# Kernel optimization log

Hardware: AMD Instinct MI355X
Metric: run time of the kernel (lower is better)

The kernel has to match this reference:

```python
import jax, jax.numpy as jnp
import numpy as np

HEAD = 16

def setup_inputs() -> dict:
    key = jax.random.key(0)
    k1, k2, k3 = jax.random.split(key, 3)
    B, S, D = 2, 2048, 1024
    x = jax.random.normal(k1, (B, S, D), dtype=jnp.float32)
    w_qkv = jax.random.normal(k2, (D, 3 * D), dtype=jnp.float32) * (1.0 / np.sqrt(D))
    b_qkv = jnp.zeros((3 * D,), dtype=jnp.float32)
    w_out = jax.random.normal(k3, (D, D), dtype=jnp.float32) * (1.0 / np.sqrt(D))
    b_out = jnp.zeros((D,), dtype=jnp.float32)
    return {"x": x, "w_qkv": w_qkv, "b_qkv": b_qkv, "w_out": w_out, "b_out": b_out}


def reference(x, w_qkv, b_qkv, w_out, b_out):
    B, S, D = x.shape
    hd = D // HEAD  # head dim
    qkv = x @ w_qkv + b_qkv                      # [B,S,3D]
    qkv = qkv.reshape(B, S, 3, HEAD, hd)
    qkv = jnp.transpose(qkv, (2, 0, 3, 1, 4))    # [3,B,H,S,hd]
    q, k, v = qkv[0], qkv[1], qkv[2]
    scores = jnp.einsum('bhqd,bhkd->bhqk', q, k)  # [B,H,S,S]
    causal = jnp.triu(jnp.ones((S, S), dtype=bool), k=1)
    scores = jnp.where(causal, -jnp.inf, scores)
    scores = scores / jnp.sqrt(jnp.asarray(hd, dtype=x.dtype))
    attn = jax.nn.softmax(scores, axis=-1)
    z = jnp.einsum('bhqk,bhkd->bhqd', attn, v)   # [B,H,S,hd]
    z = jnp.transpose(z, (0, 2, 1, 3)).reshape(B, S, D)
    out = z @ w_out + b_out
    return out
```

## Files before the change

kernel.cpp:

```cpp
#include <hip/hip_runtime.h>

#define S_LEN  2048
#define NH     16
#define HD     64
#define DMODEL 1024

using bf16x8 = __attribute__((ext_vector_type(8))) __bf16;
using f32x4  = __attribute__((ext_vector_type(4))) float;

__device__ __forceinline__ unsigned short f2bf(float f) {
    unsigned u = __float_as_uint(f);
    u += 0x7FFFu + ((u >> 16) & 1u);
    return (unsigned short)(u >> 16);
}
__device__ __forceinline__ unsigned pk_trunc(float lo, float hi) {
    return __builtin_amdgcn_perm(__float_as_uint(hi), __float_as_uint(lo), 0x07060302u);
}

#define EXP2(x) __builtin_amdgcn_exp2f(x)

#define GLDS16(gsrc, ldst) \
    __builtin_amdgcn_global_load_lds((__attribute__((address_space(1))) void*)(gsrc), \
                                     (__attribute__((address_space(3))) void*)(ldst), 16, 0, 0)

#define WAIT_LGKM0() __builtin_amdgcn_s_waitcnt(0xC07F)

#define ASM_VMCNT(n)  asm volatile("s_waitcnt vmcnt(" #n ")" ::: "memory")
#define ASM_BARRIER() asm volatile("s_barrier" ::: "memory")

__global__ __launch_bounds__(256) void prep_kernel(
    const float* __restrict__ x, const float* __restrict__ w_qkv,
    const float* __restrict__ w_out,
    unsigned short* __restrict__ xb, unsigned short* __restrict__ wqkvT,
    unsigned short* __restrict__ woutT) {
    __shared__ float T[32][33];
    int bx = blockIdx.x;
    if (bx < 4096) {
        int idx = (bx * 256 + threadIdx.x) * 4;
        float4 v = *(const float4*)(x + idx);
        ushort4 o;
        o.x = f2bf(v.x); o.y = f2bf(v.y); o.z = f2bf(v.z); o.w = f2bf(v.w);
        *(ushort4*)(xb + idx) = o;
        return;
    }
    int tb = bx - 4096;
    int tcol = tb & 127, krow = tb >> 7;
    const float* in;
    unsigned short* out;
    int N, nbx;
    if (tcol < 96) { in = w_qkv; out = wqkvT; N = 3072; nbx = tcol; }
    else           { in = w_out; out = woutT; N = 1024; nbx = tcol - 96; }
    int r  = threadIdx.x >> 3;
    int c4 = (threadIdx.x & 7) * 4;
    int kbase = krow * 32, nbase = nbx * 32;
    float4 v = *(const float4*)(in + (size_t)(kbase + r) * N + nbase + c4);
    T[r][c4 + 0] = v.x; T[r][c4 + 1] = v.y; T[r][c4 + 2] = v.z; T[r][c4 + 3] = v.w;
    __syncthreads();
    ushort4 o;
    o.x = f2bf(T[c4 + 0][r]); o.y = f2bf(T[c4 + 1][r]);
    o.z = f2bf(T[c4 + 2][r]); o.w = f2bf(T[c4 + 3][r]);
    *(ushort4*)(out + (size_t)(nbase + r) * 1024 + kbase + c4) = o;
}

template <int NI>
__device__ __forceinline__ void mfma_mainloop64(const unsigned short* __restrict__ A,
                                                const unsigned short* __restrict__ B,
                                                int K, int m0, int n0,
                                                unsigned short* As, unsigned short* Bs,
                                                f32x4 acc[4][NI]) {
    const int lane = threadIdx.x & 63, wave = threadIdx.x >> 6;
    const int quad = lane >> 4, l15 = lane & 15;
    const int wm0 = (wave >> 1) * 64, wn0 = (wave & 1) * (NI * 16);
    const int nt = K >> 6;

    auto stage = [&](int k0, int b) {
        unsigned short* Ad = As + b * 8192;
        unsigned short* Bd = Bs + b * (NI * 2048);
        #pragma unroll
        for (int j = 0; j < 4 + NI; ++j) {
            if (j < 4) {
                int c0 = j * 256 + wave * 64;
                int c  = c0 + lane;
                int r = c >> 3, pc = c & 7, q = pc ^ (r & 7);
                GLDS16(A + (size_t)(m0 + r) * K + k0 + q * 8, Ad + c0 * 8);
            } else {
                int c0 = (j - 4) * 256 + wave * 64;
                int c  = c0 + lane;
                int r = c >> 3, pc = c & 7, q = pc ^ (r & 7);
                GLDS16(B + (size_t)(n0 + r) * K + k0 + q * 8, Bd + c0 * 8);
            }
        }
    };

    auto gbody = [&](int t, int b, bool pref) {
        if (pref) {
            stage((t + 1) * 64, b ^ 1);
            if constexpr (NI == 4) { ASM_VMCNT(8); } else { ASM_VMCNT(6); }
        } else {
            ASM_VMCNT(0);
        }
        ASM_BARRIER();

        const unsigned short* Ab = As + b * 8192;
        const unsigned short* Bb = Bs + b * (NI * 2048);
        bf16x8 af[2][4], bfr[2][NI];
        #pragma unroll
        for (int mi = 0; mi < 4; ++mi) {
            int r = wm0 + mi * 16 + l15, x = r & 7;
            af[0][mi] = *(const bf16x8*)(Ab + r * 64 + ((quad    ) ^ x) * 8);
            af[1][mi] = *(const bf16x8*)(Ab + r * 64 + ((4 + quad) ^ x) * 8);
        }
        #pragma unroll
        for (int ni = 0; ni < NI; ++ni) {
            int r = wn0 + ni * 16 + l15, x = r & 7;
            bfr[0][ni] = *(const bf16x8*)(Bb + r * 64 + ((quad    ) ^ x) * 8);
            bfr[1][ni] = *(const bf16x8*)(Bb + r * 64 + ((4 + quad) ^ x) * 8);
        }
        #pragma unroll
        for (int h = 0; h < 2; ++h)
            #pragma unroll
            for (int mi = 0; mi < 4; ++mi)
                #pragma unroll
                for (int ni = 0; ni < NI; ++ni)
                    acc[mi][ni] = __builtin_amdgcn_mfma_f32_16x16x32_bf16(
                        af[h][mi], bfr[h][ni], acc[mi][ni], 0, 0, 0);
        ASM_BARRIER();
    };

    stage(0, 0);
    for (int t = 0; t < nt; t += 2) {
        gbody(t, 0, true);
        gbody(t + 1, 1, t + 2 < nt);
    }
}

__global__ __launch_bounds__(256) void gemm_qkv_kernel(
    const unsigned short* __restrict__ xb, const unsigned short* __restrict__ wT,
    const float* __restrict__ bias,
    unsigned short* __restrict__ Qt, unsigned short* __restrict__ Kh,
    unsigned short* __restrict__ Vt) {
    __shared__ __align__(16) unsigned short Sh[32768];
    unsigned short* As = Sh;
    unsigned short* Bs = Sh + 16384;

    f32x4 acc[4][4];
    #pragma unroll
    for (int i = 0; i < 4; ++i)
        #pragma unroll
        for (int j = 0; j < 4; ++j) acc[i][j] = (f32x4){0.f, 0.f, 0.f, 0.f};

    const int bid = blockIdx.x;
    const int xcd = bid & 7, slot = bid >> 3;
    const int nt = xcd * 3 + (slot % 3);
    const int mt = slot / 3;
    const int m0 = mt * 128, n0 = nt * 128;
    mfma_mainloop64<4>(xb, wT, DMODEL, m0, n0, As, Bs, acc);

    const int lane = threadIdx.x & 63, wave = threadIdx.x >> 6;
    const int quad = lane >> 4, l15 = lane & 15;
    const int wm0 = (wave >> 1) * 64, wn0 = (wave & 1) * 64;

    const int colbase = n0 + wn0;
    const int t = colbase >> 10;
    const int h = (colbase >> 6) & (NH - 1);
    const float qscale = (t == 0) ? 0.125f * 1.44269504088896f : 1.0f;
    float bv[4];
    #pragma unroll
    for (int ni = 0; ni < 4; ++ni) bv[ni] = bias[colbase + ni * 16 + l15];

    __syncthreads();
    unsigned short* Lw = Sh + wave * 1536;

    #pragma unroll
    for (int mi = 0; mi < 4; ++mi) {
        int mbase = m0 + wm0 + mi * 16;
        int b = mbase >> 11, sbase = mbase & (S_LEN - 1);
        if (t == 1) {
            #pragma unroll
            for (int ni = 0; ni < 4; ++ni)
                #pragma unroll
                for (int r = 0; r < 4; ++r)
                    Lw[(quad * 4 + r) * 72 + ni * 16 + l15] =
                        f2bf(acc[mi][ni][r] + bv[ni]);
            WAIT_LGKM0();
            int rr = lane & 15, dc = (lane >> 4) * 16;
            uint4 v0 = *(const uint4*)(Lw + rr * 72 + dc);
            uint4 v1 = *(const uint4*)(Lw + rr * 72 + dc + 8);
            unsigned short* dst =
                Kh + ((size_t)(b * NH + h) * S_LEN + sbase + rr) * HD + dc;
            *(uint4*)dst = v0;
            *(uint4*)(dst + 8) = v1;
        } else {
            #pragma unroll
            for (int ni = 0; ni < 4; ++ni)
                #pragma unroll
                for (int r = 0; r < 4; ++r)
                    Lw[(ni * 16 + l15) * 24 + quad * 4 + r] =
                        f2bf((acc[mi][ni][r] + bv[ni]) * qscale);
            WAIT_LGKM0();
            int c = lane;
            uint4 v0 = *(const uint4*)(Lw + c * 24);
            uint4 v1 = *(const uint4*)(Lw + c * 24 + 8);
            unsigned short* base = (t == 0) ? Qt : Vt;
            unsigned short* dst =
                base + ((size_t)(b * NH + h) * HD + c) * S_LEN + sbase;
            *(uint4*)dst = v0;
            *(uint4*)(dst + 8) = v1;
        }
        WAIT_LGKM0();
    }
}

__global__ __launch_bounds__(256) void gemm_out_kernel(
    const unsigned short* __restrict__ zb, const unsigned short* __restrict__ wT,
    const float* __restrict__ bias, float* __restrict__ out) {
    __shared__ __align__(16) unsigned short As[16384], Bs[8192];
    f32x4 acc[4][2];
    #pragma unroll
    for (int i = 0; i < 4; ++i)
        #pragma unroll
        for (int j = 0; j < 2; ++j) acc[i][j] = (f32x4){0.f, 0.f, 0.f, 0.f};

    const int bid = blockIdx.x;
    const int xcd = bid & 7, slot = bid >> 3;
    const int nt = xcd * 2 + (slot & 1);
    const int mt = slot >> 1;
    const int m0 = mt * 128, n0 = nt * 64;
    mfma_mainloop64<2>(zb, wT, DMODEL, m0, n0, As, Bs, acc);

    const int lane = threadIdx.x & 63, wave = threadIdx.x >> 6;
    const int quad = lane >> 4, l15 = lane & 15;
    const int wm0 = (wave >> 1) * 64, wn0 = (wave & 1) * 32;
    #pragma unroll
    for (int mi = 0; mi < 4; ++mi) {
        #pragma unroll
        for (int ni = 0; ni < 2; ++ni) {
            int col = n0 + wn0 + ni * 16 + l15;
            float bvv = bias[col];
            #pragma unroll
            for (int r = 0; r < 4; ++r)
                out[(size_t)(m0 + wm0 + mi * 16 + quad * 4 + r) * DMODEL + col] =
                    acc[mi][ni][r] + bvv;
        }
    }
}

__device__ const int g_sched[47 * 4] = {
    16,0,16,-1,
    31,0,15,0,  31,16,31,1,  30,0,15,0,  15,0,15,-1,
    30,16,30,1, 29,0,14,0,   29,15,29,1, 28,0,14,0,  14,0,14,-1,
    28,15,28,1, 27,0,13,0,   27,14,27,1, 26,0,13,0,  13,0,13,-1,
    26,14,26,1, 25,0,12,0,   25,13,25,1, 24,0,12,0,  12,0,12,-1,
    24,13,24,1, 23,0,11,0,   23,12,23,1, 22,0,11,0,  11,0,11,-1,
    22,12,22,1, 21,0,10,0,   21,11,21,1, 20,0,10,0,  10,0,10,-1,
    20,11,20,1, 19,0,9,0,    19,10,19,1, 18,0,9,0,   9,0,9,-1,
    18,10,18,1, 17,0,8,0,    17,9,17,1,  8,0,8,-1,
    7,0,7,-1, 6,0,6,-1, 5,0,5,-1, 4,0,4,-1, 3,0,3,-1, 2,0,2,-1, 1,0,1,-1, 0,0,0,-1
};

__global__ __launch_bounds__(256) void attn_mfma_kernel(
    const unsigned short* __restrict__ Qt, const unsigned short* __restrict__ Kh,
    const unsigned short* __restrict__ Vt, unsigned short* __restrict__ zb,
    float* __restrict__ Zp, float* __restrict__ lp) {
    __shared__ __align__(16) unsigned short Ks[2 * 64 * 64];
    __shared__ __align__(16) unsigned short Vs[2 * 64 * 64];
    __shared__ __align__(16) unsigned short Pl[4 * 16 * 64];

    const int lane = threadIdx.x & 63, wave = threadIdx.x >> 6;
    const int quad = lane >> 4, l15 = lane & 15;
    const int bh = blockIdx.x;
    const int qt   = g_sched[blockIdx.y * 4 + 0];
    const int klo  = g_sched[blockIdx.y * 4 + 1];
    const int khi  = g_sched[blockIdx.y * 4 + 2];
    const int part = g_sched[blockIdx.y * 4 + 3];
    const int q0 = qt * 64;
    const float M0 = 12.0f;

    bf16x8 qf0, qf1;
    {
        const unsigned short* qb = Qt + (size_t)bh * HD * S_LEN + q0 + wave * 16 + l15;
        union { bf16x8 v; unsigned short u[8]; } u0, u1;
        #pragma unroll
        for (int j = 0; j < 8; ++j) {
            u0.u[j] = qb[(quad * 8 + j) * S_LEN];
            u1.u[j] = qb[(32 + quad * 8 + j) * S_LEN];
        }
        qf0 = u0.v; qf1 = u1.v;
    }

    f32x4 Z[4];
    #pragma unroll
    for (int i = 0; i < 4; ++i) Z[i] = (f32x4){0.f, 0.f, 0.f, 0.f};
    float rsum = 0.f;

    unsigned short* pw = Pl + wave * 1024;
    const int pwrow = l15 * 64;
    const int qthr  = wave * 16 + l15 - quad * 4;

    auto stageKV = [&](int kt, int b) {
        #pragma unroll
        for (int i = 0; i < 2; ++i) {
            int c0 = (i * 4 + wave) * 64;
            int c  = c0 + lane;
            int r = c >> 3, pc = c & 7, q = pc ^ (r & 7);
            GLDS16(Kh + ((size_t)bh * S_LEN + kt * 64 + r) * HD + q * 8,
                   Ks + b * 4096 + c0 * 8);
        }
        #pragma unroll
        for (int i = 0; i < 2; ++i) {
            int c0 = (i * 4 + wave) * 64;
            int c  = c0 + lane;
            int d = c >> 3, pc = c & 7, q = pc ^ (d & 7);
            GLDS16(Vt + ((size_t)bh * HD + d) * S_LEN + kt * 64 + q * 8,
                   Vs + b * 4096 + c0 * 8);
        }
    };

    auto body = [&](int kt, int cb, bool pref) {
        if (pref) {
            stageKV(kt + 1, cb ^ 1);
            ASM_VMCNT(4);
        } else {
            ASM_VMCNT(0);
        }
        ASM_BARRIER();

        const unsigned short* Kb = Ks + cb * 4096;
        const unsigned short* Vb = Vs + cb * 4096;

        const bool diag = (kt == qt);
        const int nmax = diag ? wave : 3;

        #pragma unroll
        for (int n = 0; n < 4; ++n) {
            int woff = pwrow + (((2 * n + (quad >> 1)) ^ (l15 & 7)) << 3) + (quad & 1) * 4;
            if (n <= nmax) {
                int rk = n * 16 + l15;
                int x = rk & 7;
                bf16x8 kv0 = *(const bf16x8*)(Kb + rk * 64 + ((quad    ) ^ x) * 8);
                bf16x8 kv1 = *(const bf16x8*)(Kb + rk * 64 + ((4 + quad) ^ x) * 8);
                f32x4 t4 = (f32x4){-M0, -M0, -M0, -M0};
                __builtin_amdgcn_s_setprio(1);
                t4 = __builtin_amdgcn_mfma_f32_16x16x32_bf16(kv0, qf0, t4, 0, 0, 0);
                t4 = __builtin_amdgcn_mfma_f32_16x16x32_bf16(kv1, qf1, t4, 0, 0, 0);
                __builtin_amdgcn_s_setprio(0);
                float p[4];
                #pragma unroll
                for (int r = 0; r < 4; ++r) {
                    p[r] = EXP2(t4[r]);
                    if (diag && (n * 16 + r) > qthr) p[r] = 0.f;
                    rsum += p[r];
                }
                uint2 pk;
                pk.x = pk_trunc(p[0], p[1]);
                pk.y = pk_trunc(p[2], p[3]);
                *(uint2*)(pw + woff) = pk;
            } else {
                *(uint2*)(pw + woff) = (uint2){0u, 0u};
            }
        }

        const int khmax = diag ? (wave >> 1) : 1;
        for (int kh = 0; kh <= khmax; ++kh) {
            bf16x8 pa = *(const bf16x8*)(pw + pwrow + ((kh * 4 + quad) ^ (l15 & 7)) * 8);
            __builtin_amdgcn_s_setprio(1);
            #pragma unroll
            for (int ni = 0; ni < 4; ++ni) {
                int rd = ni * 16 + l15;
                bf16x8 vb = *(const bf16x8*)(Vb + rd * 64 + ((kh * 4 + quad) ^ (rd & 7)) * 8);
                Z[ni] = __builtin_amdgcn_mfma_f32_16x16x32_bf16(vb, pa, Z[ni], 0, 0, 0);
            }
            __builtin_amdgcn_s_setprio(0);
        }
        ASM_BARRIER();
    };

    stageKV(klo, 0);
    {
        int cnt = khi - klo + 1;
        int kt = klo;
        while (cnt >= 2) {
            body(kt, 0, true);
            body(kt + 1, 1, cnt > 2);
            kt += 2; cnt -= 2;
        }
        if (cnt == 1) body(kt, 0, false);
    }

    rsum += __shfl_xor(rsum, 16);
    rsum += __shfl_xor(rsum, 32);

    const int ql = wave * 16 + l15;
    if (part < 0) {
        const int b = bh >> 4, h = bh & (NH - 1);
        float inv = 1.f / rsum;
        size_t rowoff = (size_t)(b * S_LEN + q0 + ql) * DMODEL + h * HD;
        #pragma unroll
        for (int ni = 0; ni < 4; ++ni) {
            ushort4 o;
            o.x = f2bf(Z[ni][0] * inv);
            o.y = f2bf(Z[ni][1] * inv);
            o.z = f2bf(Z[ni][2] * inv);
            o.w = f2bf(Z[ni][3] * inv);
            *(ushort4*)(zb + rowoff + ni * 16 + quad * 4) = o;
        }
    } else {
        const int slot = (qt - 17) * 2 + part;
        float* zpo = Zp + ((size_t)(slot * 32 + bh) * 64) * 64;
        #pragma unroll
        for (int ni = 0; ni < 4; ++ni) {
            float4 st;
            st.x = Z[ni][0]; st.y = Z[ni][1]; st.z = Z[ni][2]; st.w = Z[ni][3];
            *(float4*)(zpo + (size_t)ql * 64 + ni * 16 + quad * 4) = st;
        }
        if (quad == 0)
            lp[(size_t)(slot * 32 + bh) * 64 + ql] = rsum;
    }
}

__global__ __launch_bounds__(256) void attn_merge_kernel(
    const float* __restrict__ Zp, const float* __restrict__ lp,
    unsigned short* __restrict__ zb) {
    const int bh = blockIdx.x, qi = blockIdx.y, qt = 17 + qi;
    const int t = threadIdx.x;
    const int q = t >> 2;
    const int d0 = (t & 3) << 4;
    const int s0 = qi * 2, s1 = s0 + 1;
    float l = lp[(size_t)(s0 * 32 + bh) * 64 + q] +
              lp[(size_t)(s1 * 32 + bh) * 64 + q];
    float inv = 1.f / l;
    const float* z0 = Zp + ((size_t)(s0 * 32 + bh) * 64 + q) * 64 + d0;
    const float* z1 = Zp + ((size_t)(s1 * 32 + bh) * 64 + q) * 64 + d0;
    const int b = bh >> 4, h = bh & (NH - 1);
    unsigned short* o =
        zb + (size_t)(b * S_LEN + qt * 64 + q) * DMODEL + h * HD + d0;
    #pragma unroll
    for (int i = 0; i < 16; i += 4) {
        float4 a = *(const float4*)(z0 + i);
        float4 c = *(const float4*)(z1 + i);
        ushort4 ov;
        ov.x = f2bf((a.x + c.x) * inv);
        ov.y = f2bf((a.y + c.y) * inv);
        ov.z = f2bf((a.z + c.z) * inv);
        ov.w = f2bf((a.w + c.w) * inv);
        *(ushort4*)(o + i) = ov;
    }
}

extern "C" void kernel_launch(void* const* d_in, const int* in_sizes, int n_in,
                              void* d_out, int out_size, void* d_ws, size_t ws_size,
                              hipStream_t stream)
{
    const float* x     = (const float*)d_in[0];
    const float* w_qkv = (const float*)d_in[1];
    const float* b_qkv = (const float*)d_in[2];
    const float* w_out = (const float*)d_in[3];
    const float* b_out = (const float*)d_in[4];
    float* out = (float*)d_out;

    unsigned short* wsu   = (unsigned short*)d_ws;
    unsigned short* xb    = wsu;
    unsigned short* wqkvT = xb    + (size_t)4194304;
    unsigned short* woutT = wqkvT + (size_t)3145728;
    unsigned short* Qt    = woutT + (size_t)1048576;
    unsigned short* Kh    = Qt    + (size_t)4194304;
    unsigned short* Vt    = Kh    + (size_t)4194304;
    unsigned short* zb    = Vt    + (size_t)4194304;
    float* Zp = (float*)(zb + (size_t)4194304);
    float* lp = Zp + (size_t)30 * 32 * 64 * 64;

    prep_kernel<<<dim3(8192), 256, 0, stream>>>(x, w_qkv, w_out, xb, wqkvT, woutT);

    gemm_qkv_kernel<<<dim3(768), 256, 0, stream>>>(
        xb, wqkvT, b_qkv, Qt, Kh, Vt);

    attn_mfma_kernel<<<dim3(2 * NH, 47), 256, 0, stream>>>(Qt, Kh, Vt, zb, Zp, lp);
    attn_merge_kernel<<<dim3(2 * NH, 15), 256, 0, stream>>>(Zp, lp, zb);

    gemm_out_kernel<<<dim3(512), 256, 0, stream>>>(
        zb, woutT, b_out, out);
}
```

Measured before the change: 180.0 us.

## Use 128-row query tiles with 8-wave attention blocks and rebalanced split schedule

The attention kernel now runs 512 threads per block, with each of 8 waves owning 16 query rows, so a block covers 128 queries. Each staged 64-key K/V tile is shared by twice as many query rows, which halves K/V global traffic per query. The causal schedule and the split-KV merge are rebuilt for 128-row tiles, with 24 blocks per head instead of 47. In exchange the grid is smaller (768 blocks of 512 threads), and waves whose query rows lie entirely before the diagonal sit idle through some tiles.

Result: no change. 181.5 us (+0.8%).

```diff
diff --git a/kernel.cpp b/kernel.cpp
--- a/kernel.cpp
+++ b/kernel.cpp
@@ -245,26 +245,25 @@
     }
 }
 
-__device__ const int g_sched[47 * 4] = {
-    16,0,16,-1,
-    31,0,15,0,  31,16,31,1,  30,0,15,0,  15,0,15,-1,
-    30,16,30,1, 29,0,14,0,   29,15,29,1, 28,0,14,0,  14,0,14,-1,
-    28,15,28,1, 27,0,13,0,   27,14,27,1, 26,0,13,0,  13,0,13,-1,
-    26,14,26,1, 25,0,12,0,   25,13,25,1, 24,0,12,0,  12,0,12,-1,
-    24,13,24,1, 23,0,11,0,   23,12,23,1, 22,0,11,0,  11,0,11,-1,
-    22,12,22,1, 21,0,10,0,   21,11,21,1, 20,0,10,0,  10,0,10,-1,
-    20,11,20,1, 19,0,9,0,    19,10,19,1, 18,0,9,0,   9,0,9,-1,
-    18,10,18,1, 17,0,8,0,    17,9,17,1,  8,0,8,-1,
-    7,0,7,-1, 6,0,6,-1, 5,0,5,-1, 4,0,4,-1, 3,0,3,-1, 2,0,2,-1, 1,0,1,-1, 0,0,0,-1
+__device__ const int g_sched[24 * 4] = {
+    15,0,15,0,  15,16,31,1,  7,0,15,-1,
+    14,0,14,0,  14,15,29,1,  6,0,13,-1,
+    13,0,13,0,  13,14,27,1,
+    12,0,12,0,  12,13,25,1,  5,0,11,-1,
+    11,0,11,0,  11,12,23,1,
+    10,0,10,0,  10,11,21,1,  4,0,9,-1,
+     9,0,9,0,    9,10,19,1,
+     8,0,8,0,    8,9,17,1,   3,0,7,-1,
+     2,0,5,-1,   1,0,3,-1,   0,0,1,-1
 };
 
-__global__ __launch_bounds__(256) void attn_mfma_kernel(
+__global__ __launch_bounds__(512) void attn_mfma_kernel(
     const unsigned short* __restrict__ Qt, const unsigned short* __restrict__ Kh,
     const unsigned short* __restrict__ Vt, unsigned short* __restrict__ zb,
     float* __restrict__ Zp, float* __restrict__ lp) {
     __shared__ __align__(16) unsigned short Ks[2 * 64 * 64];
     __shared__ __align__(16) unsigned short Vs[2 * 64 * 64];
-    __shared__ __align__(16) unsigned short Pl[4 * 16 * 64];
+    __shared__ __align__(16) unsigned short Pl[8 * 16 * 64];
 
     const int lane = threadIdx.x & 63, wave = threadIdx.x >> 6;
     const int quad = lane >> 4, l15 = lane & 15;
@@ -273,7 +272,7 @@
     const int klo  = g_sched[blockIdx.y * 4 + 1];
     const int khi  = g_sched[blockIdx.y * 4 + 2];
     const int part = g_sched[blockIdx.y * 4 + 3];
-    const int q0 = qt * 64;
+    const int q0 = qt * 128;
     const float M0 = 12.0f;
 
     bf16x8 qf0, qf1;
@@ -295,20 +294,17 @@
 
     unsigned short* pw = Pl + wave * 1024;
     const int pwrow = l15 * 64;
-    const int qthr  = wave * 16 + l15 - quad * 4;
 
     auto stageKV = [&](int kt, int b) {
-        #pragma unroll
-        for (int i = 0; i < 2; ++i) {
-            int c0 = (i * 4 + wave) * 64;
+        {
+            int c0 = wave * 64;
             int c  = c0 + lane;
             int r = c >> 3, pc = c & 7, q = pc ^ (r & 7);
             GLDS16(Kh + ((size_t)bh * S_LEN + kt * 64 + r) * HD + q * 8,
                    Ks + b * 4096 + c0 * 8);
         }
-        #pragma unroll
-        for (int i = 0; i < 2; ++i) {
-            int c0 = (i * 4 + wave) * 64;
+        {
+            int c0 = wave * 64;
             int c  = c0 + lane;
             int d = c >> 3, pc = c & 7, q = pc ^ (d & 7);
             GLDS16(Vt + ((size_t)bh * HD + d) * S_LEN + kt * 64 + q * 8,
@@ -319,7 +315,7 @@
     auto body = [&](int kt, int cb, bool pref) {
         if (pref) {
             stageKV(kt + 1, cb ^ 1);
-            ASM_VMCNT(4);
+            ASM_VMCNT(2);
         } else {
             ASM_VMCNT(0);
         }
@@ -328,49 +324,53 @@
         const unsigned short* Kb = Ks + cb * 4096;
         const unsigned short* Vb = Vs + cb * 4096;
 
-        const bool diag = (kt == qt);
-        const int nmax = diag ? wave : 3;
-
-        #pragma unroll
-        for (int n = 0; n < 4; ++n) {
-            int woff = pwrow + (((2 * n + (quad >> 1)) ^ (l15 & 7)) << 3) + (quad & 1) * 4;
-            if (n <= nmax) {
-                int rk = n * 16 + l15;
-                int x = rk & 7;
-                bf16x8 kv0 = *(const bf16x8*)(Kb + rk * 64 + ((quad    ) ^ x) * 8);
-                bf16x8 kv1 = *(const bf16x8*)(Kb + rk * 64 + ((4 + quad) ^ x) * 8);
-                f32x4 t4 = (f32x4){-M0, -M0, -M0, -M0};
+        const int kq = kt - 2 * qt;
+        const int dw = (kq >= 0) ? (wave - (kq << 2)) : 7;
+        if (dw >= 0) {
+            const int nmax = dw < 3 ? dw : 3;
+            const int qthr = dw * 16 + l15 - quad * 4;
+
+            #pragma unroll
+            for (int n = 0; n < 4; ++n) {
+                int woff = pwrow + (((2 * n + (quad >> 1)) ^ (l15 & 7)) << 3) + (quad & 1) * 4;
+                if (n <= nmax) {
+                    int rk = n * 16 + l15;
+                    int x = rk & 7;
+                    bf16x8 kv0 = *(const bf16x8*)(Kb + rk * 64 + ((quad    ) ^ x) * 8);
+                    bf16x8 kv1 = *(const bf16x8*)(Kb + rk * 64 + ((4 + quad) ^ x) * 8);
+                    f32x4 t4 = (f32x4){-M0, -M0, -M0, -M0};
+                    __builtin_amdgcn_s_setprio(1);
+                    t4 = __builtin_amdgcn_mfma_f32_16x16x32_bf16(kv0, qf0, t4, 0, 0, 0);
+                    t4 = __builtin_amdgcn_mfma_f32_16x16x32_bf16(kv1, qf1, t4, 0, 0, 0);
+                    __builtin_amdgcn_s_setprio(0);
+                    float p[4];
+                    #pragma unroll
+                    for (int r = 0; r < 4; ++r) {
+                        p[r] = EXP2(t4[r]);
+                        if ((n * 16 + r) > qthr) p[r] = 0.f;
+                        rsum += p[r];
+                    }
+                    uint2 pk;
+                    pk.x = pk_trunc(p[0], p[1]);
+                    pk.y = pk_trunc(p[2], p[3]);
+                    *(uint2*)(pw + woff) = pk;
+                } else {
+                    *(uint2*)(pw + woff) = (uint2){0u, 0u};
+                }
+            }
+
+            const int khmax = (dw >> 1) < 1 ? (dw >> 1) : 1;
+            for (int kh = 0; kh <= khmax; ++kh) {
+                bf16x8 pa = *(const bf16x8*)(pw + pwrow + ((kh * 4 + quad) ^ (l15 & 7)) * 8);
                 __builtin_amdgcn_s_setprio(1);
-                t4 = __builtin_amdgcn_mfma_f32_16x16x32_bf16(kv0, qf0, t4, 0, 0, 0);
-                t4 = __builtin_amdgcn_mfma_f32_16x16x32_bf16(kv1, qf1, t4, 0, 0, 0);
+                #pragma unroll
+                for (int ni = 0; ni < 4; ++ni) {
+                    int rd = ni * 16 + l15;
+                    bf16x8 vb = *(const bf16x8*)(Vb + rd * 64 + ((kh * 4 + quad) ^ (rd & 7)) * 8);
+                    Z[ni] = __builtin_amdgcn_mfma_f32_16x16x32_bf16(vb, pa, Z[ni], 0, 0, 0);
+                }
                 __builtin_amdgcn_s_setprio(0);
-                float p[4];
-                #pragma unroll
-                for (int r = 0; r < 4; ++r) {
-                    p[r] = EXP2(t4[r]);
-                    if (diag && (n * 16 + r) > qthr) p[r] = 0.f;
-                    rsum += p[r];
-                }
-                uint2 pk;
-                pk.x = pk_trunc(p[0], p[1]);
-                pk.y = pk_trunc(p[2], p[3]);
-                *(uint2*)(pw + woff) = pk;
-            } else {
-                *(uint2*)(pw + woff) = (uint2){0u, 0u};
             }
-        }
-
-        const int khmax = diag ? (wave >> 1) : 1;
-        for (int kh = 0; kh <= khmax; ++kh) {
-            bf16x8 pa = *(const bf16x8*)(pw + pwrow + ((kh * 4 + quad) ^ (l15 & 7)) * 8);
-            __builtin_amdgcn_s_setprio(1);
-            #pragma unroll
-            for (int ni = 0; ni < 4; ++ni) {
-                int rd = ni * 16 + l15;
-                bf16x8 vb = *(const bf16x8*)(Vb + rd * 64 + ((kh * 4 + quad) ^ (rd & 7)) * 8);
-                Z[ni] = __builtin_amdgcn_mfma_f32_16x16x32_bf16(vb, pa, Z[ni], 0, 0, 0);
-            }
-            __builtin_amdgcn_s_setprio(0);
         }
         ASM_BARRIER();
     };
@@ -405,37 +405,37 @@
             *(ushort4*)(zb + rowoff + ni * 16 + quad * 4) = o;
         }
     } else {
-        const int slot = (qt - 17) * 2 + part;
-        float* zpo = Zp + ((size_t)(slot * 32 + bh) * 64) * 64;
+        const int slot = (qt - 8) * 2 + part;
+        float* zpo = Zp + ((size_t)(slot * 32 + bh) * 128 + ql) * 64;
         #pragma unroll
         for (int ni = 0; ni < 4; ++ni) {
             float4 st;
             st.x = Z[ni][0]; st.y = Z[ni][1]; st.z = Z[ni][2]; st.w = Z[ni][3];
-            *(float4*)(zpo + (size_t)ql * 64 + ni * 16 + quad * 4) = st;
+            *(float4*)(zpo + ni * 16 + quad * 4) = st;
         }
         if (quad == 0)
-            lp[(size_t)(slot * 32 + bh) * 64 + ql] = rsum;
+            lp[(size_t)(slot * 32 + bh) * 128 + ql] = rsum;
     }
 }
 
 __global__ __launch_bounds__(256) void attn_merge_kernel(
     const float* __restrict__ Zp, const float* __restrict__ lp,
     unsigned short* __restrict__ zb) {
-    const int bh = blockIdx.x, qi = blockIdx.y, qt = 17 + qi;
+    const int bh = blockIdx.x, qi = blockIdx.y, qt = 8 + qi;
     const int t = threadIdx.x;
-    const int q = t >> 2;
-    const int d0 = (t & 3) << 4;
+    const int q = t >> 1;
+    const int d0 = (t & 1) << 5;
     const int s0 = qi * 2, s1 = s0 + 1;
-    float l = lp[(size_t)(s0 * 32 + bh) * 64 + q] +
-              lp[(size_t)(s1 * 32 + bh) * 64 + q];
+    float l = lp[(size_t)(s0 * 32 + bh) * 128 + q] +
+              lp[(size_t)(s1 * 32 + bh) * 128 + q];
     float inv = 1.f / l;
-    const float* z0 = Zp + ((size_t)(s0 * 32 + bh) * 64 + q) * 64 + d0;
-    const float* z1 = Zp + ((size_t)(s1 * 32 + bh) * 64 + q) * 64 + d0;
+    const float* z0 = Zp + ((size_t)(s0 * 32 + bh) * 128 + q) * 64 + d0;
+    const float* z1 = Zp + ((size_t)(s1 * 32 + bh) * 128 + q) * 64 + d0;
     const int b = bh >> 4, h = bh & (NH - 1);
     unsigned short* o =
-        zb + (size_t)(b * S_LEN + qt * 64 + q) * DMODEL + h * HD + d0;
-    #pragma unroll
-    for (int i = 0; i < 16; i += 4) {
+        zb + (size_t)(b * S_LEN + qt * 128 + q) * DMODEL + h * HD + d0;
+    #pragma unroll
+    for (int i = 0; i < 32; i += 4) {
         float4 a = *(const float4*)(z0 + i);
         float4 c = *(const float4*)(z1 + i);
         ushort4 ov;
@@ -467,15 +467,15 @@
     unsigned short* Vt    = Kh    + (size_t)4194304;
     unsigned short* zb    = Vt    + (size_t)4194304;
     float* Zp = (float*)(zb + (size_t)4194304);
-    float* lp = Zp + (size_t)30 * 32 * 64 * 64;
+    float* lp = Zp + (size_t)16 * 32 * 128 * 64;
 
     prep_kernel<<<dim3(8192), 256, 0, stream>>>(x, w_qkv, w_out, xb, wqkvT, woutT);
 
     gemm_qkv_kernel<<<dim3(768), 256, 0, stream>>>(
         xb, wqkvT, b_qkv, Qt, Kh, Vt);
 
-    attn_mfma_kernel<<<dim3(2 * NH, 47), 256, 0, stream>>>(Qt, Kh, Vt, zb, Zp, lp);
-    attn_merge_kernel<<<dim3(2 * NH, 15), 256, 0, stream>>>(Zp, lp, zb);
+    attn_mfma_kernel<<<dim3(2 * NH, 24), 512, 0, stream>>>(Qt, Kh, Vt, zb, Zp, lp);
+    attn_merge_kernel<<<dim3(2 * NH, 8), 256, 0, stream>>>(Zp, lp, zb);
 
     gemm_out_kernel<<<dim3(512), 256, 0, stream>>>(
         zb, woutT, b_out, out);
```
